# Kernel optimization log

Hardware: AMD Instinct MI355X
Metric: run time of the kernel (lower is better)

The kernel has to match this reference:

```python
import jax, jax.numpy as jnp
import numpy as np

N, K = 4096, 12          # nodes, incoming edges per node
E = N * K                # bonds
INPUT_DIM = 128
N_HEADS = 16
HEAD_DIM = 8
OUT_DIM = N_HEADS * HEAD_DIM   # 128
NUM_GAUSS = 20
NUM_ANG_FUNCS = 3              # AngularEncoding -> 1 + 3*2*2 = 13 dims
A_DIM = 1 + NUM_ANG_FUNCS * 4
KV_DIM = INPUT_DIM + 2 * NUM_GAUSS + A_DIM  # 181
Q_DIM = INPUT_DIM


def _build_graph_and_triplets():
    # edge e = i*K + t-1 : row=(i+t)%N -> col=i  (K incoming edges per node)
    col = np.repeat(np.arange(N), K)
    row = (col + np.tile(np.arange(1, K + 1), N)) % N
    bond_index = np.stack([row, col]).astype(np.int64)  # [2, E]
    # triplets: for edge e=(j->i), pair with every incoming edge (k->j) of j
    idx_ji = np.repeat(np.arange(E), K)
    idx_kj = np.repeat(row, K) * K + np.tile(np.arange(K), E)
    idx_i = col[idx_ji]
    idx_j = row[idx_ji]
    idx_k = row[idx_kj]
    mask = idx_i != idx_k
    return (bond_index, idx_i[mask], idx_j[mask], idx_k[mask],
            idx_kj[mask], idx_ji[mask])


def setup_inputs() -> dict:
    key = jax.random.key(0)
    ks = jax.random.split(key, 8)
    bond_index, idx_i, idx_j, idx_k, idx_kj, idx_ji = _build_graph_and_triplets()
    w = 0.05
    return {
        "h": jax.random.normal(ks[0], (N, INPUT_DIM), dtype=jnp.float32),
        "h_bond": jax.random.normal(ks[1], (E, INPUT_DIM), dtype=jnp.float32),
        "pos": jax.random.normal(ks[2], (N, 3), dtype=jnp.float32),
        "bond_index": jnp.asarray(bond_index),
        "idx_i": jnp.asarray(idx_i), "idx_j": jnp.asarray(idx_j),
        "idx_k": jnp.asarray(idx_k), "idx_kj": jnp.asarray(idx_kj),
        "idx_ji": jnp.asarray(idx_ji),
        "W_key": jax.random.normal(ks[3], (KV_DIM, OUT_DIM), dtype=jnp.float32) * w,
        "W_value": jax.random.normal(ks[4], (KV_DIM, OUT_DIM), dtype=jnp.float32) * w,
        "W_query": jax.random.normal(ks[5], (Q_DIM, OUT_DIM), dtype=jnp.float32) * w,
        "W_edge0": jax.random.normal(ks[6], (NUM_GAUSS, OUT_DIM), dtype=jnp.float32) * w,
        "W_edge1": jax.random.normal(ks[7], (NUM_GAUSS, OUT_DIM), dtype=jnp.float32) * w,
    }


def reference(h, h_bond, pos, bond_index, idx_i, idx_j, idx_k, idx_kj, idx_ji,
              W_key, W_value, W_query, W_edge0, W_edge1):
    Eb = h_bond.shape[0]
    row, col = bond_index[0], bond_index[1]
    # per-bond distance + Gaussian smearing (start=0, stop=10, 20 gaussians)
    dist = jnp.sqrt(jnp.sum((pos[col] - pos[row]) ** 2, axis=-1))  # [E]
    offset = jnp.linspace(0.0, 10.0, NUM_GAUSS)
    coeff = -0.5 / (offset[1] - offset[0]) ** 2
    r_feat = jnp.exp(coeff * (dist[:, None] - offset) ** 2)        # [E, 20]
    # per-triplet angle + angular encoding
    pos_i = pos[idx_i]
    pos_ji = pos[idx_j] - pos_i
    pos_ki = pos[idx_k] - pos_i
    a = jnp.sum(pos_ji * pos_ki, axis=-1)
    b = jnp.linalg.norm(jnp.cross(pos_ji, pos_ki), axis=-1)
    angle = jnp.arctan2(b, a)                                      # [T]
    t = jnp.arange(1, NUM_ANG_FUNCS + 1, dtype=jnp.float32)
    freq = jnp.concatenate([t, 1.0 / t])                           # [6]
    x = angle[:, None]
    a_feat = jnp.concatenate([x, jnp.sin(x * freq), jnp.cos(x * freq)], axis=-1)  # [T,13]
    # triplet gathers
    r_kj, r_ji = r_feat[idx_kj], r_feat[idx_ji]
    kv_input = jnp.concatenate([h_bond[idx_kj], r_kj, r_ji, a_feat], axis=-1)  # [T,181]
    q_input = h_bond[idx_ji]                                                    # [T,128]
    T = kv_input.shape[0]
    k_proj = (kv_input @ W_key).reshape(T, N_HEADS, HEAD_DIM)
    v_proj = (kv_input @ W_value).reshape(T, N_HEADS, HEAD_DIM)
    q_proj = (q_input @ W_query).reshape(T, N_HEADS, HEAD_DIM)
    edge_attn = jnp.tanh(r_ji @ W_edge0).reshape(T, N_HEADS, HEAD_DIM)
    alpha = jnp.sum(q_proj * k_proj * edge_attn, axis=-1) / np.sqrt(HEAD_DIM)   # [T,H]
    # segment softmax over idx_ji (torch_geometric softmax semantics)
    m = jax.lax.stop_gradient(jax.ops.segment_max(alpha, idx_ji, num_segments=Eb))
    ex = jnp.exp(alpha - m[idx_ji])
    s = jax.ops.segment_sum(ex, idx_ji, num_segments=Eb)
    alpha = ex / (s[idx_ji] + 1e-16)
    msg = v_proj * jnp.tanh(r_ji @ W_edge1).reshape(T, N_HEADS, HEAD_DIM)
    msg = msg * alpha[:, :, None]
    out = jax.ops.segment_sum(msg, idx_ji, num_segments=Eb)  # [E,H,D]
    return out.reshape(Eb, OUT_DIM)
```

## Files before the change

### kernel.cpp

```cpp
#include <hip/hip_runtime.h>
#include <math.h>

#define INPUT_DIM 128
#define OUT_DIM 128
#define NUM_GAUSS 20
#define NH 16
#define BM 64
#define MAXT 16
#define WPB 4
#define SCALE 0.35355339059327373f


static __device__ __forceinline__ void wave_lds_fence() {
    __asm__ volatile("s_waitcnt lgkmcnt(0)" ::: "memory");
    __builtin_amdgcn_wave_barrier();
}

__global__ __launch_bounds__(256) void rbf_kernel(
    const float* __restrict__ pos,
    const int*   __restrict__ bond_index,
    float* __restrict__ r_out,
    int E)
{
    int e = blockIdx.x * 256 + threadIdx.x;
    if (e >= E) return;
    int jrow = bond_index[e];
    int icol = bond_index[E + e];
    float dx = pos[icol*3+0] - pos[jrow*3+0];
    float dy = pos[icol*3+1] - pos[jrow*3+1];
    float dz = pos[icol*3+2] - pos[jrow*3+2];
    float dist = sqrtf(dx*dx + dy*dy + dz*dz);
    const float step = 10.f / (NUM_GAUSS - 1);
    const float coeff = -0.5f / (step * step);
    float v[NUM_GAUSS];
    #pragma unroll
    for (int g = 0; g < NUM_GAUSS; ++g) {
        float t = dist - g * step;
        v[g] = __expf(coeff * t * t);
    }
    float4* o = (float4*)&r_out[(size_t)e * NUM_GAUSS];
    #pragma unroll
    for (int q = 0; q < 5; ++q)
        o[q] = make_float4(v[4*q], v[4*q+1], v[4*q+2], v[4*q+3]);
}

__global__ __launch_bounds__(256, 3) void bond_proj_kernel(
    const float* __restrict__ h_bond,
    const float* __restrict__ r_feat,
    const float* __restrict__ Wk,
    const float* __restrict__ Wv,
    const float* __restrict__ Wq,
    const float* __restrict__ We0,
    float* __restrict__ KB,
    float* __restrict__ VB,
    float* __restrict__ QE,
    int E)
{
    __shared__ float As[BM * 148];
    const int tid = threadIdx.x;
    const int e0 = blockIdx.x * BM;

    for (int i = tid; i < BM * 32; i += 256) {
        int e = i >> 5, c = (i & 31) << 2;
        float4 v = make_float4(0.f, 0.f, 0.f, 0.f);
        if (e0 + e < E) v = *(const float4*)&h_bond[(size_t)(e0 + e) * INPUT_DIM + c];
        float* dst = &As[e * 148 + c];
        dst[0] = v.x; dst[1] = v.y; dst[2] = v.z; dst[3] = v.w;
    }
    for (int i = tid; i < BM * 5; i += 256) {
        int e = i / 5, q = (i % 5) << 2;
        float4 v = make_float4(0.f, 0.f, 0.f, 0.f);
        if (e0 + e < E) v = *(const float4*)&r_feat[(size_t)(e0 + e) * NUM_GAUSS + q];
        float* dst = &As[e * 148 + 128 + q];
        dst[0] = v.x; dst[1] = v.y; dst[2] = v.z; dst[3] = v.w;
    }
    __syncthreads();

    const int em = tid >> 5;
    const int dn = (tid & 31) << 2;
    const float* AsB = &As[em * 8 * 148];

    float aK[8][4], aV[8][4], aQ[8][4], aE[8][4];
    #pragma unroll
    for (int m = 0; m < 8; ++m)
        #pragma unroll
        for (int j = 0; j < 4; ++j) { aK[m][j]=0.f; aV[m][j]=0.f; aQ[m][j]=0.f; aE[m][j]=0.f; }

    #pragma unroll 2
    for (int c = 0; c < 128; ++c) {
        float4 wk = *(const float4*)&Wk[c * OUT_DIM + dn];
        float4 wv = *(const float4*)&Wv[c * OUT_DIM + dn];
        float4 wq = *(const float4*)&Wq[c * OUT_DIM + dn];
        #pragma unroll
        for (int m = 0; m < 8; ++m) {
            float a = AsB[m * 148 + c];
            aK[m][0] = fmaf(a, wk.x, aK[m][0]); aK[m][1] = fmaf(a, wk.y, aK[m][1]);
            aK[m][2] = fmaf(a, wk.z, aK[m][2]); aK[m][3] = fmaf(a, wk.w, aK[m][3]);
            aV[m][0] = fmaf(a, wv.x, aV[m][0]); aV[m][1] = fmaf(a, wv.y, aV[m][1]);
            aV[m][2] = fmaf(a, wv.z, aV[m][2]); aV[m][3] = fmaf(a, wv.w, aV[m][3]);
            aQ[m][0] = fmaf(a, wq.x, aQ[m][0]); aQ[m][1] = fmaf(a, wq.y, aQ[m][1]);
            aQ[m][2] = fmaf(a, wq.z, aQ[m][2]); aQ[m][3] = fmaf(a, wq.w, aQ[m][3]);
        }
    }
    #pragma unroll 2
    for (int g = 0; g < 20; ++g) {
        float4 wk = *(const float4*)&Wk[(INPUT_DIM + g) * OUT_DIM + dn];
        float4 wv = *(const float4*)&Wv[(INPUT_DIM + g) * OUT_DIM + dn];
        float4 w0 = *(const float4*)&We0[g * OUT_DIM + dn];
        #pragma unroll
        for (int m = 0; m < 8; ++m) {
            float a = AsB[m * 148 + 128 + g];
            aK[m][0] = fmaf(a, wk.x, aK[m][0]); aK[m][1] = fmaf(a, wk.y, aK[m][1]);
            aK[m][2] = fmaf(a, wk.z, aK[m][2]); aK[m][3] = fmaf(a, wk.w, aK[m][3]);
            aV[m][0] = fmaf(a, wv.x, aV[m][0]); aV[m][1] = fmaf(a, wv.y, aV[m][1]);
            aV[m][2] = fmaf(a, wv.z, aV[m][2]); aV[m][3] = fmaf(a, wv.w, aV[m][3]);
            aE[m][0] = fmaf(a, w0.x, aE[m][0]); aE[m][1] = fmaf(a, w0.y, aE[m][1]);
            aE[m][2] = fmaf(a, w0.z, aE[m][2]); aE[m][3] = fmaf(a, w0.w, aE[m][3]);
        }
    }

    #pragma unroll
    for (int m = 0; m < 8; ++m) {
        int e = e0 + em * 8 + m;
        if (e < E) {
            *(float4*)&KB[(size_t)e * OUT_DIM + dn] =
                make_float4(aK[m][0], aK[m][1], aK[m][2], aK[m][3]);
            *(float4*)&VB[(size_t)e * OUT_DIM + dn] =
                make_float4(aV[m][0], aV[m][1], aV[m][2], aV[m][3]);
            *(float4*)&QE[(size_t)e * OUT_DIM + dn] =
                make_float4(aQ[m][0] * tanhf(aE[m][0]), aQ[m][1] * tanhf(aE[m][1]),
                            aQ[m][2] * tanhf(aE[m][2]), aQ[m][3] * tanhf(aE[m][3]));
        }
    }
}

__global__ __launch_bounds__(256) void redge_kernel(
    const float* __restrict__ r_feat,
    const float* __restrict__ QE,
    const float* __restrict__ Wk,
    const float* __restrict__ Wv,
    const float* __restrict__ We1,
    float* __restrict__ EA1,
    float* __restrict__ ERV,
    float* __restrict__ QRK2,
    int E)
{
    __shared__ float Rs[BM][NUM_GAUSS];
    const int tid = threadIdx.x;
    const int e0 = blockIdx.x * BM;

    for (int i = tid; i < BM * 5; i += 256) {
        int e = i / 5, q = (i % 5) << 2;
        float4 v = make_float4(0.f, 0.f, 0.f, 0.f);
        if (e0 + e < E) v = *(const float4*)&r_feat[(size_t)(e0 + e) * NUM_GAUSS + q];
        Rs[e][q] = v.x; Rs[e][q+1] = v.y; Rs[e][q+2] = v.z; Rs[e][q+3] = v.w;
    }
    __syncthreads();

    const int em = tid >> 5;
    const int dn = (tid & 31) << 2;

    {
        float a1[8][4], aS[8][4];
        #pragma unroll
        for (int m = 0; m < 8; ++m)
            #pragma unroll
            for (int j = 0; j < 4; ++j) { a1[m][j] = 0.f; aS[m][j] = 0.f; }

        #pragma unroll 2
        for (int g = 0; g < 20; ++g) {
            float4 w1 = *(const float4*)&We1[g * OUT_DIM + dn];
            float4 wv = *(const float4*)&Wv[(148 + g) * OUT_DIM + dn];
            #pragma unroll
            for (int m = 0; m < 8; ++m) {
                float a = Rs[em * 8 + m][g];
                a1[m][0] = fmaf(a, w1.x, a1[m][0]); a1[m][1] = fmaf(a, w1.y, a1[m][1]);
                a1[m][2] = fmaf(a, w1.z, a1[m][2]); a1[m][3] = fmaf(a, w1.w, a1[m][3]);
                aS[m][0] = fmaf(a, wv.x, aS[m][0]); aS[m][1] = fmaf(a, wv.y, aS[m][1]);
                aS[m][2] = fmaf(a, wv.z, aS[m][2]); aS[m][3] = fmaf(a, wv.w, aS[m][3]);
            }
        }
        #pragma unroll
        for (int m = 0; m < 8; ++m) {
            int e = e0 + em * 8 + m;
            if (e < E) {
                float t0 = tanhf(a1[m][0]), t1 = tanhf(a1[m][1]);
                float t2 = tanhf(a1[m][2]), t3 = tanhf(a1[m][3]);
                *(float4*)&EA1[(size_t)e * OUT_DIM + dn] = make_float4(t0, t1, t2, t3);
                *(float4*)&ERV[(size_t)e * OUT_DIM + dn] =
                    make_float4(t0 * aS[m][0], t1 * aS[m][1], t2 * aS[m][2], t3 * aS[m][3]);
            }
        }
    }

    {
        float aR[8][4];
        #pragma unroll
        for (int m = 0; m < 8; ++m)
            #pragma unroll
            for (int j = 0; j < 4; ++j) aR[m][j] = 0.f;

        #pragma unroll 2
        for (int g = 0; g < 20; ++g) {
            float4 wk = *(const float4*)&Wk[(148 + g) * OUT_DIM + dn];
            #pragma unroll
            for (int m = 0; m < 8; ++m) {
                float a = Rs[em * 8 + m][g];
                aR[m][0] = fmaf(a, wk.x, aR[m][0]); aR[m][1] = fmaf(a, wk.y, aR[m][1]);
                aR[m][2] = fmaf(a, wk.z, aR[m][2]); aR[m][3] = fmaf(a, wk.w, aR[m][3]);
            }
        }
        const int hh = (tid & 31) >> 1;
        #pragma unroll
        for (int m = 0; m < 8; ++m) {
            int e = e0 + em * 8 + m;
            float s = 0.f;
            if (e < E) {
                float4 q = *(const float4*)&QE[(size_t)e * OUT_DIM + dn];
                s = q.x*aR[m][0] + q.y*aR[m][1] + q.z*aR[m][2] + q.w*aR[m][3];
            }
            s += __shfl_xor(s, 1);
            if ((tid & 1) == 0 && e < E) QRK2[(size_t)e * NH + hh] = s;
        }
    }
}

__global__ __launch_bounds__(256) void attn_wave_kernel(
    const float* __restrict__ pos,
    const int*   __restrict__ idx_i,
    const int*   __restrict__ idx_j,
    const int*   __restrict__ idx_k,
    const float* __restrict__ Wk,
    const float* __restrict__ Wv,
    const float* __restrict__ KB,
    const float* __restrict__ VB,
    const float* __restrict__ QE,
    const float* __restrict__ EA1,
    const float* __restrict__ ERV,
    const float* __restrict__ QRK2,
    float* __restrict__ out,
    int E)
{
    __shared__ float afL[WPB][2][12][13];

    unsigned bid = blockIdx.x, nwg = gridDim.x;
    unsigned qq = nwg >> 3, rr = nwg & 7, xc = bid & 7, rest = bid >> 3;
    unsigned swz = (xc < rr ? xc * (qq + 1) : rr * (qq + 1) + (xc - rr) * qq) + rest;

    const int l = threadIdx.x & 63;
    const int wvn = __builtin_amdgcn_readfirstlane(threadIdx.x >> 6);
    const int sg = l >> 5;
    const int s  = l & 31;
    const int e = (int)swz * (WPB * 2) + wvn * 2 + sg;
    if (e >= E) return;
    const int h = s >> 1;
    const int a = s & 1;
    const int d4 = 4 * s;

    const int ii = idx_i[(size_t)e * 12];
    const int jj = idx_j[(size_t)e * 12];
    const size_t kjb = (size_t)jj * 12;

    const float4 qe4  = *(const float4*)&QE [(size_t)e * OUT_DIM + d4];
    const float4 ea4  = *(const float4*)&EA1[(size_t)e * OUT_DIM + d4];
    const float4 erv4 = *(const float4*)&ERV[(size_t)e * OUT_DIM + d4];
    const float qrk2 = QRK2[(size_t)e * NH + h];

    const float pix = pos[ii*3+0], piy = pos[ii*3+1], piz = pos[ii*3+2];
    const float jx = pos[jj*3+0]-pix, jy = pos[jj*3+1]-piy, jz = pos[jj*3+2]-piz;
    if (s < 12) {
        int kk = idx_k[(size_t)e * 12 + s];
        float kx = pos[kk*3+0]-pix, ky = pos[kk*3+1]-piy, kz = pos[kk*3+2]-piz;
        float aa = jx*kx + jy*ky + jz*kz;
        float cx = jy*kz - jz*ky, cy = jz*kx - jx*kz, cz = jx*ky - jy*kx;
        float bb = sqrtf(cx*cx + cy*cy + cz*cz);
        float ang = atan2f(bb, aa);
        float af0[13];
        af0[0] = ang;
        const float fr[6] = {1.f, 2.f, 3.f, 1.f, 0.5f, 1.f/3.f};
        #pragma unroll
        for (int q = 0; q < 6; ++q)
            __sincosf(ang * fr[q], &af0[1+q], &af0[7+q]);
        #pragma unroll
        for (int c = 0; c < 13; ++c) afL[wvn][sg][s][c] = af0[c];
    }

    float qwk[13];
    #pragma unroll
    for (int c = 0; c < 13; ++c) {
        float4 w = *(const float4*)&Wk[(168 + c) * OUT_DIM + d4];
        float p = qe4.x*w.x + qe4.y*w.y + qe4.z*w.z + qe4.w*w.w;
        p += __shfl_xor(p, 1);
        qwk[c] = p;
    }

    float qk6[6];
    #pragma unroll
    for (int t = 0; t < 12; ++t) {
        float4 kb = *(const float4*)&KB[(kjb + t) * OUT_DIM + d4];
        float v = qe4.x*kb.x + qe4.y*kb.y + qe4.z*kb.z + qe4.w*kb.w;
        v += __shfl_xor(v, 1);
        if ((t & 1) == a) qk6[t >> 1] = v;
    }

    wave_lds_fence();

    float lg[6];
    #pragma unroll
    for (int q = 0; q < 6; ++q) {
        int t = 2*q + a;
        float ang = 0.f;
        #pragma unroll
        for (int c = 0; c < 13; ++c) ang = fmaf(afL[wvn][sg][t][c], qwk[c], ang);
        lg[q] = (qk6[q] + ang + qrk2) * SCALE;
    }

    float m = lg[0];
    #pragma unroll
    for (int q = 1; q < 6; ++q) m = fmaxf(m, lg[q]);
    m = fmaxf(m, __shfl_xor(m, 1));
    float ex[6], ss = 0.f;
    #pragma unroll
    for (int q = 0; q < 6; ++q) { ex[q] = __expf(lg[q] - m); ss += ex[q]; }
    ss += __shfl_xor(ss, 1);
    float inv = 1.f / (ss + 1e-16f);
    float al[6], alp[6];
    #pragma unroll
    for (int q = 0; q < 6; ++q) { al[q] = ex[q] * inv; alp[q] = __shfl_xor(al[q], 1); }
    float Sh = ss * inv;

    float waf[13];
    #pragma unroll
    for (int c = 0; c < 13; ++c) {
        float wp = 0.f;
        #pragma unroll
        for (int q = 0; q < 6; ++q) wp = fmaf(al[q], afL[wvn][sg][2*q + a][c], wp);
        wp += __shfl_xor(wp, 1);
        waf[c] = wp;
    }

    float ac0 = 0.f, ac1 = 0.f, ac2 = 0.f, ac3 = 0.f;
    #pragma unroll
    for (int t = 0; t < 12; ++t) {
        float4 vb = *(const float4*)&VB[(kjb + t) * OUT_DIM + d4];
        float at = ((t & 1) == a) ? al[t >> 1] : alp[t >> 1];
        ac0 = fmaf(at, vb.x, ac0); ac1 = fmaf(at, vb.y, ac1);
        ac2 = fmaf(at, vb.z, ac2); ac3 = fmaf(at, vb.w, ac3);
    }

    float vA0 = 0.f, vA1 = 0.f, vA2 = 0.f, vA3 = 0.f;
    #pragma unroll
    for (int c = 0; c < 13; ++c) {
        float4 w = *(const float4*)&Wv[(168 + c) * OUT_DIM + d4];
        vA0 = fmaf(waf[c], w.x, vA0); vA1 = fmaf(waf[c], w.y, vA1);
        vA2 = fmaf(waf[c], w.z, vA2); vA3 = fmaf(waf[c], w.w, vA3);
    }

    float4 o;
    o.x = ea4.x * (ac0 + vA0) + erv4.x * Sh;
    o.y = ea4.y * (ac1 + vA1) + erv4.y * Sh;
    o.z = ea4.z * (ac2 + vA2) + erv4.z * Sh;
    o.w = ea4.w * (ac3 + vA3) + erv4.w * Sh;
    *(float4*)&out[(size_t)e * OUT_DIM + d4] = o;
}

__global__ __launch_bounds__(128) void attn_generic_kernel(
    const float* __restrict__ pos,
    const int*   __restrict__ idx_i,
    const int*   __restrict__ idx_j,
    const int*   __restrict__ idx_k,
    const int*   __restrict__ idx_kj,
    const int*   __restrict__ idx_ji,
    const float* __restrict__ Wk,
    const float* __restrict__ Wv,
    const float* __restrict__ We1,
    const float* __restrict__ r_feat,
    const float* __restrict__ KB,
    const float* __restrict__ VB,
    const float* __restrict__ QE,
    float* __restrict__ out,
    int E, int T)
{
    __shared__ float rs[NUM_GAUSS];
    __shared__ float af[MAXT][13];
    __shared__ float logit[MAXT][NH];
    __shared__ float qwk[NH][13];
    __shared__ float waf[NH][13];
    __shared__ int   kjs[MAXT];
    __shared__ float qrk2s[NH];
    __shared__ float Shs[NH];

    const int e = blockIdx.x;
    const int d = threadIdx.x;
    const int h8 = d >> 3;

    int l = 0, hi = T;
    while (l < hi) { int mid = (l + hi) >> 1; if (idx_ji[mid] < e) l = mid + 1; else hi = mid; }
    int lo = l, c2 = 0;
    while (lo + c2 < T && c2 < MAXT && idx_ji[lo + c2] == e) ++c2;
    int cnt = c2;

    if (d < NUM_GAUSS) rs[d] = r_feat[(size_t)e * NUM_GAUSS + d];
    if (d < cnt) {
        int t = lo + d;
        kjs[d] = idx_kj[t];
        int ii = idx_i[t], jj = idx_j[t], kk = idx_k[t];
        float pix = pos[ii*3+0], piy = pos[ii*3+1], piz = pos[ii*3+2];
        float jx = pos[jj*3+0]-pix, jy = pos[jj*3+1]-piy, jz = pos[jj*3+2]-piz;
        float kx = pos[kk*3+0]-pix, ky = pos[kk*3+1]-piy, kz = pos[kk*3+2]-piz;
        float aa = jx*kx + jy*ky + jz*kz;
        float cx = jy*kz - jz*ky, cy = jz*kx - jx*kz, cz = jx*ky - jy*kx;
        float bb = sqrtf(cx*cx + cy*cy + cz*cz);
        float ang = atan2f(bb, aa);
        af[d][0] = ang;
        const float fr[6] = {1.f, 2.f, 3.f, 1.f, 0.5f, 1.f/3.f};
        #pragma unroll
        for (int q = 0; q < 6; ++q) {
            float s, cc;
            __sincosf(ang * fr[q], &s, &cc);
            af[d][1 + q] = s;
            af[d][7 + q] = cc;
        }
    }
    __syncthreads();

    const float qe = QE[(size_t)e * OUT_DIM + d];
    float s1 = 0.f, sk = 0.f, sv = 0.f;
    #pragma unroll
    for (int g = 0; g < NUM_GAUSS; ++g) {
        float rg = rs[g];
        s1 = fmaf(rg, We1[g * OUT_DIM + d], s1);
        sk = fmaf(rg, Wk[(148 + g) * OUT_DIM + d], sk);
        sv = fmaf(rg, Wv[(148 + g) * OUT_DIM + d], sv);
    }
    const float ea1 = tanhf(s1);
    const float rv2 = sv;

    {
        float v = qe * sk;
        v += __shfl_xor(v, 1, 8); v += __shfl_xor(v, 2, 8); v += __shfl_xor(v, 4, 8);
        if ((d & 7) == 0) qrk2s[h8] = v;
    }
    {
        float p[13];
        #pragma unroll
        for (int c = 0; c < 13; ++c) p[c] = qe * Wk[(168 + c) * OUT_DIM + d];
        #pragma unroll
        for (int c = 0; c < 13; ++c) {
            float v = p[c];
            v += __shfl_xor(v, 1, 8); v += __shfl_xor(v, 2, 8); v += __shfl_xor(v, 4, 8);
            if ((d & 7) == 0) qwk[h8][c] = v;
        }
    }
    for (int t = 0; t < cnt; ++t) {
        float lv = qe * KB[(size_t)kjs[t] * OUT_DIM + d];
        lv += __shfl_xor(lv, 1, 8); lv += __shfl_xor(lv, 2, 8); lv += __shfl_xor(lv, 4, 8);
        if ((d & 7) == 0) logit[t][h8] = lv;
    }
    __syncthreads();
    {
        const int hh = d & 15;
        for (int t = d >> 4; t < cnt; t += 8) {
            float s = 0.f;
            #pragma unroll
            for (int c = 0; c < 13; ++c) s = fmaf(af[t][c], qwk[hh][c], s);
            logit[t][hh] = (logit[t][hh] + s + qrk2s[hh]) * SCALE;
        }
    }
    __syncthreads();
    if (d < NH) {
        float m = -1e30f;
        for (int t = 0; t < cnt; ++t) m = fmaxf(m, logit[t][d]);
        float s = 0.f;
        for (int t = 0; t < cnt; ++t) { float ex = __expf(logit[t][d] - m); logit[t][d] = ex; s += ex; }
        float inv = 1.f / (s + 1e-16f);
        for (int t = 0; t < cnt; ++t) logit[t][d] *= inv;
        Shs[d] = s * inv;
    }
    __syncthreads();
    {
        const int hh = d & 15;
        int c = d >> 4;
        float w1 = 0.f;
        for (int t = 0; t < cnt; ++t) w1 = fmaf(logit[t][hh], af[t][c], w1);
        waf[hh][c] = w1;
        c += 8;
        if (c < 13) {
            float w2 = 0.f;
            for (int t = 0; t < cnt; ++t) w2 = fmaf(logit[t][hh], af[t][c], w2);
            waf[hh][c] = w2;
        }
    }
    __syncthreads();
    float vA = 0.f;
    #pragma unroll
    for (int c = 0; c < 13; ++c) vA = fmaf(waf[h8][c], Wv[(168 + c) * OUT_DIM + d], vA);
    float acc = 0.f;
    for (int t = 0; t < cnt; ++t)
        acc = fmaf(logit[t][h8], VB[(size_t)kjs[t] * OUT_DIM + d], acc);
    out[(size_t)e * OUT_DIM + d] = ea1 * (acc + vA + rv2 * Shs[h8]);
}

extern "C" void kernel_launch(void* const* d_in, const int* in_sizes, int n_in,
                              void* d_out, int out_size, void* d_ws, size_t ws_size,
                              hipStream_t stream) {
    const float* h_bond = (const float*)d_in[1];
    const float* pos    = (const float*)d_in[2];
    const int*   bidx   = (const int*)d_in[3];
    const int*   idx_i  = (const int*)d_in[4];
    const int*   idx_j  = (const int*)d_in[5];
    const int*   idx_k  = (const int*)d_in[6];
    const int*   idx_kj = (const int*)d_in[7];
    const int*   idx_ji = (const int*)d_in[8];
    const float* Wk     = (const float*)d_in[9];
    const float* Wv     = (const float*)d_in[10];
    const float* Wq     = (const float*)d_in[11];
    const float* We0    = (const float*)d_in[12];
    const float* We1    = (const float*)d_in[13];

    const int E = in_sizes[1] / INPUT_DIM;
    const int T = in_sizes[4];

    float* ws = (float*)d_ws;
    float* r_feat = ws;
    float* KB   = r_feat + (size_t)E * NUM_GAUSS;
    float* VB   = KB   + (size_t)E * OUT_DIM;
    float* QE   = VB   + (size_t)E * OUT_DIM;
    float* EA1  = QE   + (size_t)E * OUT_DIM;
    float* ERV  = EA1  + (size_t)E * OUT_DIM;
    float* QRK2 = ERV  + (size_t)E * OUT_DIM;

    rbf_kernel<<<(E + 255) / 256, 256, 0, stream>>>(pos, bidx, r_feat, E);

    bond_proj_kernel<<<(E + BM - 1) / BM, 256, 0, stream>>>(
        h_bond, r_feat, Wk, Wv, Wq, We0, KB, VB, QE, E);

    redge_kernel<<<(E + BM - 1) / BM, 256, 0, stream>>>(
        r_feat, QE, Wk, Wv, We1, EA1, ERV, QRK2, E);

    if (T == E * 12) {
        const int segs_per_block = WPB * 2;
        attn_wave_kernel<<<(E + segs_per_block - 1) / segs_per_block, 64 * WPB, 0, stream>>>(
            pos, idx_i, idx_j, idx_k,
            Wk, Wv, KB, VB, QE, EA1, ERV, QRK2, (float*)d_out, E);
    } else {
        attn_generic_kernel<<<E, 128, 0, stream>>>(
            pos, idx_i, idx_j, idx_k, idx_kj, idx_ji,
            Wk, Wv, We1, r_feat, KB, VB, QE, (float*)d_out, E, T);
    }
}
```

Measured before the change: 164.6 us.

## Fuse RBF into bond projection and fold redge work into attention kernel

The separate RBF kernel is merged into bond_proj_kernel, which now computes the Gaussian features itself, writing them to shared memory and to global r_feat. The redge kernel is removed. Its per-edge tanh(r@We1), value r-term and key r-term dot product are recomputed inside attn_wave_kernel from r_feat and the weight rows, removing two launches and the EA1/ERV/QRK2 intermediate buffers. The cost is redundant distance computation per Gaussian element in bond_proj and more per-lane loads and FMAs (20 iterations of three float4 weight loads) in the attention kernel.

```diff
diff --git a/kernel.cpp b/kernel.cpp
--- a/kernel.cpp
+++ b/kernel.cpp
@@ -16,41 +16,15 @@
     __builtin_amdgcn_wave_barrier();
 }
 
-__global__ __launch_bounds__(256) void rbf_kernel(
+__global__ __launch_bounds__(256, 3) void bond_proj_kernel(
+    const float* __restrict__ h_bond,
     const float* __restrict__ pos,
     const int*   __restrict__ bond_index,
-    float* __restrict__ r_out,
-    int E)
-{
-    int e = blockIdx.x * 256 + threadIdx.x;
-    if (e >= E) return;
-    int jrow = bond_index[e];
-    int icol = bond_index[E + e];
-    float dx = pos[icol*3+0] - pos[jrow*3+0];
-    float dy = pos[icol*3+1] - pos[jrow*3+1];
-    float dz = pos[icol*3+2] - pos[jrow*3+2];
-    float dist = sqrtf(dx*dx + dy*dy + dz*dz);
-    const float step = 10.f / (NUM_GAUSS - 1);
-    const float coeff = -0.5f / (step * step);
-    float v[NUM_GAUSS];
-    #pragma unroll
-    for (int g = 0; g < NUM_GAUSS; ++g) {
-        float t = dist - g * step;
-        v[g] = __expf(coeff * t * t);
-    }
-    float4* o = (float4*)&r_out[(size_t)e * NUM_GAUSS];
-    #pragma unroll
-    for (int q = 0; q < 5; ++q)
-        o[q] = make_float4(v[4*q], v[4*q+1], v[4*q+2], v[4*q+3]);
-}
-
-__global__ __launch_bounds__(256, 3) void bond_proj_kernel(
-    const float* __restrict__ h_bond,
-    const float* __restrict__ r_feat,
     const float* __restrict__ Wk,
     const float* __restrict__ Wv,
     const float* __restrict__ Wq,
     const float* __restrict__ We0,
+    float* __restrict__ r_out,
     float* __restrict__ KB,
     float* __restrict__ VB,
     float* __restrict__ QE,
@@ -67,12 +41,26 @@
         float* dst = &As[e * 148 + c];
         dst[0] = v.x; dst[1] = v.y; dst[2] = v.z; dst[3] = v.w;
     }
-    for (int i = tid; i < BM * 5; i += 256) {
-        int e = i / 5, q = (i % 5) << 2;
-        float4 v = make_float4(0.f, 0.f, 0.f, 0.f);
-        if (e0 + e < E) v = *(const float4*)&r_feat[(size_t)(e0 + e) * NUM_GAUSS + q];
-        float* dst = &As[e * 148 + 128 + q];
-        dst[0] = v.x; dst[1] = v.y; dst[2] = v.z; dst[3] = v.w;
+    {
+        const float step = 10.f / (NUM_GAUSS - 1);
+        const float coeff = -0.5f / (step * step);
+        for (int i = tid; i < BM * NUM_GAUSS; i += 256) {
+            int e = i / NUM_GAUSS, g = i % NUM_GAUSS;
+            int ge = e0 + e;
+            float rv = 0.f;
+            if (ge < E) {
+                int jrow = bond_index[ge];
+                int icol = bond_index[E + ge];
+                float dx = pos[icol*3+0] - pos[jrow*3+0];
+                float dy = pos[icol*3+1] - pos[jrow*3+1];
+                float dz = pos[icol*3+2] - pos[jrow*3+2];
+                float dist = sqrtf(dx*dx + dy*dy + dz*dz);
+                float t = dist - g * step;
+                rv = __expf(coeff * t * t);
+                r_out[(size_t)ge * NUM_GAUSS + g] = rv;
+            }
+            As[e * 148 + 128 + g] = rv;
+        }
     }
     __syncthreads();
 
@@ -134,97 +122,6 @@
     }
 }
 
-__global__ __launch_bounds__(256) void redge_kernel(
-    const float* __restrict__ r_feat,
-    const float* __restrict__ QE,
-    const float* __restrict__ Wk,
-    const float* __restrict__ Wv,
-    const float* __restrict__ We1,
-    float* __restrict__ EA1,
-    float* __restrict__ ERV,
-    float* __restrict__ QRK2,
-    int E)
-{
-    __shared__ float Rs[BM][NUM_GAUSS];
-    const int tid = threadIdx.x;
-    const int e0 = blockIdx.x * BM;
-
-    for (int i = tid; i < BM * 5; i += 256) {
-        int e = i / 5, q = (i % 5) << 2;
-        float4 v = make_float4(0.f, 0.f, 0.f, 0.f);
-        if (e0 + e < E) v = *(const float4*)&r_feat[(size_t)(e0 + e) * NUM_GAUSS + q];
-        Rs[e][q] = v.x; Rs[e][q+1] = v.y; Rs[e][q+2] = v.z; Rs[e][q+3] = v.w;
-    }
-    __syncthreads();
-
-    const int em = tid >> 5;
-    const int dn = (tid & 31) << 2;
-
-    {
-        float a1[8][4], aS[8][4];
-        #pragma unroll
-        for (int m = 0; m < 8; ++m)
-            #pragma unroll
-            for (int j = 0; j < 4; ++j) { a1[m][j] = 0.f; aS[m][j] = 0.f; }
-
-        #pragma unroll 2
-        for (int g = 0; g < 20; ++g) {
-            float4 w1 = *(const float4*)&We1[g * OUT_DIM + dn];
-            float4 wv = *(const float4*)&Wv[(148 + g) * OUT_DIM + dn];
-            #pragma unroll
-            for (int m = 0; m < 8; ++m) {
-                float a = Rs[em * 8 + m][g];
-                a1[m][0] = fmaf(a, w1.x, a1[m][0]); a1[m][1] = fmaf(a, w1.y, a1[m][1]);
-                a1[m][2] = fmaf(a, w1.z, a1[m][2]); a1[m][3] = fmaf(a, w1.w, a1[m][3]);
-                aS[m][0] = fmaf(a, wv.x, aS[m][0]); aS[m][1] = fmaf(a, wv.y, aS[m][1]);
-                aS[m][2] = fmaf(a, wv.z, aS[m][2]); aS[m][3] = fmaf(a, wv.w, aS[m][3]);
-            }
-        }
-        #pragma unroll
-        for (int m = 0; m < 8; ++m) {
-            int e = e0 + em * 8 + m;
-            if (e < E) {
-                float t0 = tanhf(a1[m][0]), t1 = tanhf(a1[m][1]);
-                float t2 = tanhf(a1[m][2]), t3 = tanhf(a1[m][3]);
-                *(float4*)&EA1[(size_t)e * OUT_DIM + dn] = make_float4(t0, t1, t2, t3);
-                *(float4*)&ERV[(size_t)e * OUT_DIM + dn] =
-                    make_float4(t0 * aS[m][0], t1 * aS[m][1], t2 * aS[m][2], t3 * aS[m][3]);
-            }
-        }
-    }
-
-    {
-        float aR[8][4];
-        #pragma unroll
-        for (int m = 0; m < 8; ++m)
-            #pragma unroll
-            for (int j = 0; j < 4; ++j) aR[m][j] = 0.f;
-
-        #pragma unroll 2
-        for (int g = 0; g < 20; ++g) {
-            float4 wk = *(const float4*)&Wk[(148 + g) * OUT_DIM + dn];
-            #pragma unroll
-            for (int m = 0; m < 8; ++m) {
-                float a = Rs[em * 8 + m][g];
-                aR[m][0] = fmaf(a, wk.x, aR[m][0]); aR[m][1] = fmaf(a, wk.y, aR[m][1]);
-                aR[m][2] = fmaf(a, wk.z, aR[m][2]); aR[m][3] = fmaf(a, wk.w, aR[m][3]);
-            }
-        }
-        const int hh = (tid & 31) >> 1;
-        #pragma unroll
-        for (int m = 0; m < 8; ++m) {
-            int e = e0 + em * 8 + m;
-            float s = 0.f;
-            if (e < E) {
-                float4 q = *(const float4*)&QE[(size_t)e * OUT_DIM + dn];
-                s = q.x*aR[m][0] + q.y*aR[m][1] + q.z*aR[m][2] + q.w*aR[m][3];
-            }
-            s += __shfl_xor(s, 1);
-            if ((tid & 1) == 0 && e < E) QRK2[(size_t)e * NH + hh] = s;
-        }
-    }
-}
-
 __global__ __launch_bounds__(256) void attn_wave_kernel(
     const float* __restrict__ pos,
     const int*   __restrict__ idx_i,
@@ -232,12 +129,11 @@
     const int*   __restrict__ idx_k,
     const float* __restrict__ Wk,
     const float* __restrict__ Wv,
+    const float* __restrict__ We1,
+    const float* __restrict__ r_feat,
     const float* __restrict__ KB,
     const float* __restrict__ VB,
     const float* __restrict__ QE,
-    const float* __restrict__ EA1,
-    const float* __restrict__ ERV,
-    const float* __restrict__ QRK2,
     float* __restrict__ out,
     int E)
 {
@@ -261,10 +157,31 @@
     const int jj = idx_j[(size_t)e * 12];
     const size_t kjb = (size_t)jj * 12;
 
-    const float4 qe4  = *(const float4*)&QE [(size_t)e * OUT_DIM + d4];
-    const float4 ea4  = *(const float4*)&EA1[(size_t)e * OUT_DIM + d4];
-    const float4 erv4 = *(const float4*)&ERV[(size_t)e * OUT_DIM + d4];
-    const float qrk2 = QRK2[(size_t)e * NH + h];
+    const float4 qe4 = *(const float4*)&QE[(size_t)e * OUT_DIM + d4];
+
+    float a1x=0.f,a1y=0.f,a1z=0.f,a1w=0.f;
+    float arx=0.f,ary=0.f,arz=0.f,arw=0.f;
+    float avx=0.f,avy=0.f,avz=0.f,avw=0.f;
+    {
+        const float* rp = &r_feat[(size_t)e * NUM_GAUSS];
+        #pragma unroll
+        for (int g = 0; g < NUM_GAUSS; ++g) {
+            float rg = rp[g];
+            float4 w1  = *(const float4*)&We1[g * OUT_DIM + d4];
+            float4 wkr = *(const float4*)&Wk[(148 + g) * OUT_DIM + d4];
+            float4 wvr = *(const float4*)&Wv[(148 + g) * OUT_DIM + d4];
+            a1x = fmaf(rg, w1.x, a1x); a1y = fmaf(rg, w1.y, a1y);
+            a1z = fmaf(rg, w1.z, a1z); a1w = fmaf(rg, w1.w, a1w);
+            arx = fmaf(rg, wkr.x, arx); ary = fmaf(rg, wkr.y, ary);
+            arz = fmaf(rg, wkr.z, arz); arw = fmaf(rg, wkr.w, arw);
+            avx = fmaf(rg, wvr.x, avx); avy = fmaf(rg, wvr.y, avy);
+            avz = fmaf(rg, wvr.z, avz); avw = fmaf(rg, wvr.w, avw);
+        }
+    }
+    float4 ea4 = make_float4(tanhf(a1x), tanhf(a1y), tanhf(a1z), tanhf(a1w));
+    float4 erv4 = make_float4(ea4.x * avx, ea4.y * avy, ea4.z * avz, ea4.w * avw);
+    float qrk2 = qe4.x*arx + qe4.y*ary + qe4.z*arz + qe4.w*arw;
+    qrk2 += __shfl_xor(qrk2, 1);
 
     const float pix = pos[ii*3+0], piy = pos[ii*3+1], piz = pos[ii*3+2];
     const float jx = pos[jj*3+0]-pix, jy = pos[jj*3+1]-piy, jz = pos[jj*3+2]-piz;
@@ -523,26 +440,18 @@
 
     float* ws = (float*)d_ws;
     float* r_feat = ws;
-    float* KB   = r_feat + (size_t)E * NUM_GAUSS;
-    float* VB   = KB   + (size_t)E * OUT_DIM;
-    float* QE   = VB   + (size_t)E * OUT_DIM;
-    float* EA1  = QE   + (size_t)E * OUT_DIM;
-    float* ERV  = EA1  + (size_t)E * OUT_DIM;
-    float* QRK2 = ERV  + (size_t)E * OUT_DIM;
-
-    rbf_kernel<<<(E + 255) / 256, 256, 0, stream>>>(pos, bidx, r_feat, E);
+    float* KB = r_feat + (size_t)E * NUM_GAUSS;
+    float* VB = KB + (size_t)E * OUT_DIM;
+    float* QE = VB + (size_t)E * OUT_DIM;
 
     bond_proj_kernel<<<(E + BM - 1) / BM, 256, 0, stream>>>(
-        h_bond, r_feat, Wk, Wv, Wq, We0, KB, VB, QE, E);
-
-    redge_kernel<<<(E + BM - 1) / BM, 256, 0, stream>>>(
-        r_feat, QE, Wk, Wv, We1, EA1, ERV, QRK2, E);
+        h_bond, pos, bidx, Wk, Wv, Wq, We0, r_feat, KB, VB, QE, E);
 
     if (T == E * 12) {
         const int segs_per_block = WPB * 2;
         attn_wave_kernel<<<(E + segs_per_block - 1) / segs_per_block, 64 * WPB, 0, stream>>>(
             pos, idx_i, idx_j, idx_k,
-            Wk, Wv, KB, VB, QE, EA1, ERV, QRK2, (float*)d_out, E);
+            Wk, Wv, We1, r_feat, KB, VB, QE, (float*)d_out, E);
     } else {
         attn_generic_kernel<<<E, 128, 0, stream>>>(
             pos, idx_i, idx_j, idx_k, idx_kj, idx_ji,
```

After: 223.6 us. 1.36x slower.
